# Performance work log

Measured on AMD Instinct MI355X. Metric: run time of the kernel, lower is better.

The kernel has to match this reference:

```python
import jax, jax.numpy as jnp
import numpy as np

B = 1024          # batch of users
N_ITEMS = 100000  # catalog size
N_CLUSTERS = 10   # __init__ default num_clusters
D = 64            # low-rank dim of the inner recommender


def setup_inputs() -> dict:
    key = jax.random.key(0)
    k1, k2, k3, k4 = jax.random.split(key, 4)
    input_array = jax.random.uniform(k1, (B, N_CLUSTERS), dtype=jnp.float32)
    # partition of items into clusters (dense form of cluster_to_items / item_to_cluster)
    item_cluster = jax.random.randint(k2, (N_ITEMS,), 0, N_CLUSTERS, dtype=jnp.int64 if jax.config.jax_enable_x64 else jnp.int32)
    W1 = jax.random.normal(k3, (N_ITEMS, D), dtype=jnp.float32) * 0.02
    W2 = jax.random.normal(k4, (D, N_ITEMS), dtype=jnp.float32) * 0.02
    return {"input_array": input_array, "item_cluster": item_cluster, "W1": W1, "W2": W2}


def reference(input_array, item_cluster, W1, W2):
    # scatter cluster score to every item in the cluster == gather by item's cluster id
    user_vector = input_array[:, item_cluster]                 # [B, N_ITEMS]
    logits = (user_vector @ W1) @ W2                           # inner recommender, [B, N_ITEMS]
    probs = jax.nn.softmax(logits, axis=1)                     # [B, N_ITEMS]
    # per-user, per-cluster mean of item probabilities (segment mean over items)
    counts = jax.ops.segment_sum(jnp.ones((item_cluster.shape[0],), probs.dtype),
                                 item_cluster, num_segments=N_CLUSTERS)  # [N_CLUSTERS]
    sums = jax.ops.segment_sum(probs.T, item_cluster, num_segments=N_CLUSTERS).T  # [B, N_CLUSTERS]
    return sums / jnp.maximum(counts, 1.0)[None, :]            # empty cluster -> 0.0, as in source
```

## Files before the change

### kernel.cpp

```cpp
#include <hip/hip_runtime.h>
#include <hip/hip_bf16.h>

#define N_B 1024
#define N_ITEMS 100000
#define N_CLUSTERS 10
#define N_D 64
#define MAXT 6272
#define K1B 392
#define W2PB 1563
#define K3BY 48
#define NGW 192

typedef __attribute__((ext_vector_type(8))) short short8;
typedef __attribute__((ext_vector_type(4))) float f32x4;

#if defined(__has_builtin)
#if __has_builtin(__builtin_amdgcn_exp2f)
#define EXP2F(x) __builtin_amdgcn_exp2f(x)
#endif
#endif
#ifndef EXP2F
#define EXP2F(x) exp2f(x)
#endif

#define MFMA(a, b, c) __builtin_amdgcn_mfma_f32_16x16x32_bf16(a, b, c, 0, 0, 0)

__device__ __forceinline__ unsigned short bf16_rne(float x) {
  unsigned u = __float_as_uint(x);
  u += 0x7FFFu + ((u >> 16) & 1u);
  return (unsigned short)(u >> 16);
}
__device__ __forceinline__ float bf16_f(unsigned short b) {
  return __uint_as_float(((unsigned)b) << 16);
}

__global__ __launch_bounds__(256) void kA(
    const int* __restrict__ cl, const float* __restrict__ W1,
    const float* __restrict__ W2, float* __restrict__ S1p,
    float* __restrict__ cntp, int* __restrict__ inv,
    unsigned short* __restrict__ W2Ph, unsigned short* __restrict__ W2Pl) {
  __shared__ float smem[64 * 65];
  int t = threadIdx.x;
  if (blockIdx.x < K1B) {
    float (*s1)[N_CLUSTERS][N_D] = (float (*)[N_CLUSTERS][N_D])smem;
    float (*scnt)[N_CLUSTERS] =
        (float (*)[N_CLUSTERS])(smem + 4 * N_CLUSTERS * N_D);
    int wave = t >> 6, lane = t & 63;

    inv[blockIdx.x * 256 + t] = 0;

    float a[N_CLUSTERS], cn[N_CLUSTERS];
#pragma unroll
    for (int k = 0; k < N_CLUSTERS; ++k) { a[k] = 0.f; cn[k] = 0.f; }

    int gw = blockIdx.x * 4 + wave;
    int r0 = gw * 64;
#pragma unroll 1
    for (int b = 0; b < 8; ++b) {
      int i0 = r0 + b * 8;
      float w[8];
      int c[8];
      if (i0 + 8 <= N_ITEMS) {
#pragma unroll
        for (int j = 0; j < 8; ++j) {
          c[j] = cl[i0 + j];
          w[j] = W1[(size_t)(i0 + j) * N_D + lane];
        }
      } else {
#pragma unroll
        for (int j = 0; j < 8; ++j) {
          int i = i0 + j;
          bool ok = i < N_ITEMS;
          c[j] = ok ? cl[i] : -1;
          w[j] = ok ? W1[(size_t)i * N_D + lane] : 0.f;
        }
      }
#pragma unroll
      for (int j = 0; j < 8; ++j)
#pragma unroll
        for (int k = 0; k < N_CLUSTERS; ++k) {
          bool m = (c[j] == k);
          a[k] += m ? w[j] : 0.f;
          cn[k] += m ? 1.f : 0.f;
        }
    }
#pragma unroll
    for (int k = 0; k < N_CLUSTERS; ++k) s1[wave][k][lane] = a[k];
    if (lane == 0) {
#pragma unroll
      for (int k = 0; k < N_CLUSTERS; ++k) scnt[wave][k] = cn[k];
    }
    __syncthreads();
    const float* fs1 = smem;
    for (int i = t; i < N_CLUSTERS * N_D; i += 256) {
      S1p[blockIdx.x * 640 + i] =
          fs1[i] + fs1[640 + i] + fs1[1280 + i] + fs1[1920 + i];
    }
    if (t < N_CLUSTERS) {
      cntp[blockIdx.x * N_CLUSTERS + t] =
          scnt[0][t] + scnt[1][t] + scnt[2][t] + scnt[3][t];
    }
  } else {
    float (*tile)[65] = (float (*)[65])smem;
    int blk = blockIdx.x - K1B;
    int c0 = blk * 64;
    int cl_ = t & 63;
    int r0 = t >> 6;
    bool okr = (c0 + cl_) < N_ITEMS;
#pragma unroll
    for (int rr = 0; rr < 16; ++rr) {
      int r = rr * 4 + r0;
      tile[cl_][r] = okr ? W2[(size_t)r * N_ITEMS + c0 + cl_] : 0.f;
    }
    __syncthreads();
#pragma unroll
    for (int itw = 0; itw < 8; ++itw) {
      int task = itw * 256 + t;
      int c_l = task >> 5, dp = task & 31;
      int c = c0 + c_l;
      if (c < N_ITEMS) {
        float v0 = tile[c_l][dp * 2], v1 = tile[c_l][dp * 2 + 1];
        unsigned short h0 = bf16_rne(v0), h1 = bf16_rne(v1);
        unsigned short l0 = bf16_rne(v0 - bf16_f(h0));
        unsigned short l1 = bf16_rne(v1 - bf16_f(h1));
        ((unsigned*)W2Ph)[(size_t)c * 32 + dp] =
            (unsigned)h0 | ((unsigned)h1 << 16);
        ((unsigned*)W2Pl)[(size_t)c * 32 + dp] =
            (unsigned)l0 | ((unsigned)l1 << 16);
      }
    }
  }
}

__global__ __launch_bounds__(256) void k1r(
    const float* __restrict__ S1p, const float* __restrict__ cntp,
    float* __restrict__ S1g, float* __restrict__ cntF, int* __restrict__ meta,
    int* __restrict__ tinfo, int* __restrict__ cursor) {
  int t = threadIdx.x;
  if (blockIdx.x > 0) {
    __shared__ float sgp[4][64];
    int wave = t >> 6, lane = t & 63;
    int col = (blockIdx.x - 1) * 64 + lane;
    float s = 0.f;
    const float* sp = S1p + col;
#pragma unroll 4
    for (int b = wave; b < K1B; b += 4) s += sp[b * 640];
    sgp[wave][lane] = s;
    __syncthreads();
    if (t < 64) {
      S1g[(blockIdx.x - 1) * 64 + t] =
          sgp[0][t] + sgp[1][t] + sgp[2][t] + sgp[3][t];
    }
    return;
  }
  __shared__ int baseS[11];
  __shared__ int cntI[N_CLUSTERS];
  __shared__ float part[16][N_CLUSTERS];
  if (t < 16) cursor[t] = 0;
  if (t < 160) {
    int c = t % N_CLUSTERS, g = t / N_CLUSTERS;
    float s = 0.f;
    for (int b = g; b < K1B; b += 16) s += cntp[b * N_CLUSTERS + c];
    part[g][c] = s;
  }
  __syncthreads();
  if (t < N_CLUSTERS) {
    float s = 0.f;
#pragma unroll
    for (int g = 0; g < 16; ++g) s += part[g][t];
    cntF[t] = s;
    cntI[t] = (int)(s + 0.5f);
  }
  __syncthreads();
  if (t == 0) {
    int acc = 0;
    for (int c = 0; c < N_CLUSTERS; ++c) {
      baseS[c] = acc;
      acc += ((cntI[c] + 15) >> 4) << 4;
    }
    baseS[10] = acc;
    for (int c = 0; c < 11; ++c) meta[c] = baseS[c];
    meta[11] = acc >> 4;
  }
  __syncthreads();
  int NT = baseS[10] >> 4;
  for (int jt = t; jt < MAXT; jt += 256) {
    int c = 0, nv = 0;
    if (jt < NT) {
      int p0 = jt * 16;
      for (int k = 0; k < N_CLUSTERS; ++k)
        if (p0 >= baseS[k] && p0 < baseS[k + 1]) c = k;
      nv = min(16, cntI[c] - (p0 - baseS[c]));
      if (nv < 0) nv = 0;
    }
    tinfo[jt] = c | (nv << 8);
  }
}

__global__ __launch_bounds__(256) void kB(
    const int* __restrict__ cl, const int* __restrict__ meta,
    int* __restrict__ cursor, int* __restrict__ inv,
    const float* __restrict__ inp, const float* __restrict__ S1g,
    short8* __restrict__ hfrag, float* __restrict__ bucket) {
  __shared__ int wn[4][N_CLUSTERS];
  __shared__ int bb[N_CLUSTERS];
  int t = threadIdx.x;
  if (blockIdx.x < 391) {
    int i = blockIdx.x * 256 + t;
    if (i < N_B * N_CLUSTERS) bucket[i] = 0.f;
    int wave = t >> 6, lane = t & 63;
    int c = (i < N_ITEMS) ? cl[i] : -1;
    unsigned long long m[N_CLUSTERS];
#pragma unroll
    for (int k = 0; k < N_CLUSTERS; ++k) {
      m[k] = __ballot(c == k);
      if (lane == 0) wn[wave][k] = __popcll(m[k]);
    }
    __syncthreads();
    if (t < N_CLUSTERS) {
      int tot = wn[0][t] + wn[1][t] + wn[2][t] + wn[3][t];
      bb[t] = tot ? atomicAdd(&cursor[t], tot) : 0;
    }
    __syncthreads();
    if (c >= 0) {
      int rank = 0;
#pragma unroll
      for (int k = 0; k < N_CLUSTERS; ++k)
        if (c == k) rank = __popcll(m[k] & ((1ull << lane) - 1ull));
      int wsum = 0;
      for (int w2 = 0; w2 < wave; ++w2) wsum += wn[w2][c];
      inv[meta[c] + bb[c] + wsum + rank] = i;
    }
  } else {
    int id = (blockIdx.x - 391) * 256 + t;
    int lane = id & 63;
    int ks = (id >> 6) & 1;
    int rt = (id >> 7) & 3;
    int bx = id >> 9;
    int row = bx * 64 + rt * 16 + (lane & 15);
    int d0 = ks * 32 + (lane >> 4) * 8;
    float hv[8];
#pragma unroll
    for (int j = 0; j < 8; ++j) hv[j] = 0.f;
#pragma unroll
    for (int c = 0; c < N_CLUSTERS; ++c) {
      float ic = inp[row * N_CLUSTERS + c];
      const float* sp = S1g + c * N_D + d0;
#pragma unroll
      for (int j = 0; j < 8; ++j) hv[j] += ic * sp[j];
    }
    short8 hi8, lo8;
#pragma unroll
    for (int j = 0; j < 8; ++j) {
      float x = hv[j] * 1.44269504088896340736f;
      unsigned short us = bf16_rne(x);
      hi8[j] = (short)us;
      lo8[j] = (short)bf16_rne(x - bf16_f(us));
    }
    int f0 = rt * 4 + ks * 2;
    hfrag[(bx * 16 + f0) * 64 + lane] = hi8;
    hfrag[(bx * 16 + f0 + 1) * 64 + lane] = lo8;
  }
}

__global__ __launch_bounds__(256, 3) void k3_mfma(
    const unsigned short* __restrict__ W2Ph,
    const unsigned short* __restrict__ W2Pl,
    const short8* __restrict__ hfrag, const int* __restrict__ inv,
    const int* __restrict__ tinfo, float* __restrict__ bucket) {
  __shared__ int linv[4][544];
  int t = threadIdx.x;
  int wave = t >> 6, lane = t & 63;
  int l15 = lane & 15, quad = lane >> 4;

  int lid = blockIdx.y * 16 + blockIdx.x;
  int nid = (lid & 7) * 96 + (lid >> 3);
  int bx = nid & 15, by = nid >> 4;

  int gw = by * 4 + wave;
  int jt0 = (MAXT * gw) / NGW;
  int nt = (MAXT * (gw + 1)) / NGW - jt0;

  short8 fr[16];
  {
    const short8* hp = hfrag + bx * 1024 + lane;
#pragma unroll
    for (int f = 0; f < 16; ++f) fr[f] = hp[f * 64];
  }
  int tiv = tinfo[jt0 + ((lane < nt) ? lane : nt - 1)];
  {
    const int* ip = inv + jt0 * 16;
    int n = nt * 16;
    for (int i = lane; i < n; i += 64) linv[wave][i] = ip[i];
  }
  __syncthreads();

  f32x4 acc[4];
#pragma unroll
  for (int r = 0; r < 4; ++r) acc[r] = (f32x4){0.f, 0.f, 0.f, 0.f};

  short8 xh0, xl0, xh1, xl1, yh0, yl0, yh1, yl1;
  int cc, nv, colN;
  {
    int c0 = inv[jt0 * 16 + l15];
    int o = c0 * 64 + quad * 8;
    xh0 = *(const short8*)(W2Ph + o);
    xh1 = *(const short8*)(W2Ph + o + 32);
    xl0 = *(const short8*)(W2Pl + o);
    xl1 = *(const short8*)(W2Pl + o + 32);
    colN = inv[jt0 * 16 + 16 + l15];
    int ti = __builtin_amdgcn_readlane(tiv, 0);
    cc = ti & 255;
    nv = ti >> 8;
  }

#define K3_FLUSH()                                                            \
  {                                                                           \
    _Pragma("unroll") for (int rt = 0; rt < 4; ++rt) {                        \
      float e0 = acc[rt][0], e1 = acc[rt][1];                                 \
      float e2 = acc[rt][2], e3 = acc[rt][3];                                 \
      _Pragma("unroll") for (int mm = 1; mm < 16; mm <<= 1) {                 \
        e0 += __shfl_xor(e0, mm, 64);                                         \
        e1 += __shfl_xor(e1, mm, 64);                                         \
        e2 += __shfl_xor(e2, mm, 64);                                         \
        e3 += __shfl_xor(e3, mm, 64);                                         \
      }                                                                       \
      if (l15 == 0) {                                                         \
        int r = bx * 64 + rt * 16 + quad * 4;                                 \
        atomicAdd(&bucket[(r + 0) * N_CLUSTERS + cc], e0);                    \
        atomicAdd(&bucket[(r + 1) * N_CLUSTERS + cc], e1);                    \
        atomicAdd(&bucket[(r + 2) * N_CLUSTERS + cc], e2);                    \
        atomicAdd(&bucket[(r + 3) * N_CLUSTERS + cc], e3);                    \
      }                                                                       \
      acc[rt] = (f32x4){0.f, 0.f, 0.f, 0.f};                                  \
    }                                                                         \
  }

#define K3_PHASE(CH0, CL0, CH1, CL1, NH0, NL0, NH1, NL1)                      \
  {                                                                           \
    int tin = __builtin_amdgcn_readlane(tiv, (it + 1 < nt) ? it + 1 : nt - 1);\
    int ccn = tin & 255, nvn = tin >> 8;                                      \
    {                                                                         \
      int o = colN * 64 + quad * 8;                   \
      NH0 = *(const short8*)(W2Ph + o);                                       \
      NH1 = *(const short8*)(W2Ph + o + 32);                                  \
      NL0 = *(const short8*)(W2Pl + o);                                       \
      NL1 = *(const short8*)(W2Pl + o + 32);                                  \
    }                                                                         \
    colN = linv[wave][((it + 2 < nt) ? it + 2 : nt - 1) * 16 + l15];          \
    f32x4 cr[4];                                                              \
    _Pragma("unroll") for (int rt = 0; rt < 4; ++rt) {                        \
      f32x4 c = {0.f, 0.f, 0.f, 0.f};                                         \
      c = MFMA(fr[rt * 4 + 0], CH0, c);                                       \
      c = MFMA(fr[rt * 4 + 0], CL0, c);                                       \
      c = MFMA(fr[rt * 4 + 1], CH0, c);                                       \
      c = MFMA(fr[rt * 4 + 2], CH1, c);                                       \
      c = MFMA(fr[rt * 4 + 2], CL1, c);                                       \
      c = MFMA(fr[rt * 4 + 3], CH1, c);                                       \
      cr[rt] = c;                                                             \
    }                                                                         \
    if (nv == 16) {                                                           \
      _Pragma("unroll") for (int rt = 0; rt < 4; ++rt) {                      \
        acc[rt][0] += EXP2F(cr[rt][0]);                                       \
        acc[rt][1] += EXP2F(cr[rt][1]);                                       \
        acc[rt][2] += EXP2F(cr[rt][2]);                                       \
        acc[rt][3] += EXP2F(cr[rt][3]);                                       \
      }                                                                       \
    } else {                                                                  \
      _Pragma("unroll") for (int rt = 0; rt < 4; ++rt) {                      \
        acc[rt][0] += (l15 < nv) ? EXP2F(cr[rt][0]) : 0.f;                    \
        acc[rt][1] += (l15 < nv) ? EXP2F(cr[rt][1]) : 0.f;                    \
        acc[rt][2] += (l15 < nv) ? EXP2F(cr[rt][2]) : 0.f;                    \
        acc[rt][3] += (l15 < nv) ? EXP2F(cr[rt][3]) : 0.f;                    \
      }                                                                       \
    }                                                                         \
    if (it == nt - 1 || ccn != cc) K3_FLUSH();                                \
    cc = ccn;                                                                 \
    nv = nvn;                                                                 \
    ++it;                                                                     \
    if (it == nt) break;                                                      \
  }

  int it = 0;
  while (true) {
    K3_PHASE(xh0, xl0, xh1, xl1, yh0, yl0, yh1, yl1)
    K3_PHASE(yh0, yl0, yh1, yl1, xh0, xl0, xh1, xl1)
  }
#undef K3_PHASE
#undef K3_FLUSH
}

__global__ __launch_bounds__(320) void k4_fin(
    const float* __restrict__ bucket, const float* __restrict__ cntF,
    float* __restrict__ out) {
  __shared__ float bl[32][N_CLUSTERS];
  int t = threadIdx.x;
  int r = t / N_CLUSTERS, c = t % N_CLUSTERS;
  int row = blockIdx.x * 32 + r;
  float s = bucket[row * N_CLUSTERS + c];
  bl[r][c] = s;
  __syncthreads();
  float tot = 0.f;
#pragma unroll
  for (int k = 0; k < N_CLUSTERS; ++k) tot += bl[r][k];
  out[row * N_CLUSTERS + c] = s / (tot * fmaxf(cntF[c], 1.f));
}

extern "C" void kernel_launch(void* const* d_in, const int* in_sizes, int n_in,
                              void* d_out, int out_size, void* d_ws, size_t ws_size,
                              hipStream_t stream) {
  const float* input = (const float*)d_in[0];
  const int* cl      = (const int*)d_in[1];
  const float* W1    = (const float*)d_in[2];
  const float* W2    = (const float*)d_in[3];
  float* out = (float*)d_out;
  float* ws = (float*)d_ws;

  float* S1g            = ws;
  float* cntF           = ws + 640;
  int*   meta           = (int*)(ws + 656);
  int*   cursor         = (int*)(ws + 672);
  int*   tinfo          = (int*)(ws + 1024);
  int*   inv            = (int*)(ws + 16384);
  short8* hfrag         = (short8*)(ws + 131072);
  unsigned short* W2Ph  = (unsigned short*)(ws + 262144);
  unsigned short* W2Pl  = (unsigned short*)(ws + 3463168);
  float* S1p            = ws + 6664192;
  float* cntp           = ws + 6915072;
  float* bucket         = ws + 6918992;

  kA<<<K1B + W2PB, 256, 0, stream>>>(cl, W1, W2, S1p, cntp, inv, W2Ph, W2Pl);
  k1r<<<11, 256, 0, stream>>>(S1p, cntp, S1g, cntF, meta, tinfo, cursor);
  kB<<<391 + 32, 256, 0, stream>>>(cl, meta, cursor, inv, input, S1g, hfrag,
                                   bucket);
  dim3 g3(16, K3BY);
  k3_mfma<<<g3, 256, 0, stream>>>(W2Ph, W2Pl, hfrag, inv, tinfo, bucket);
  k4_fin<<<32, 320, 0, stream>>>(bucket, cntF, out);
}
```

Before: 179.2 us.

## Hand-schedule W2 prefetch loads with inline asm and explicit vmcnt waits

```diff
diff --git a/kernel.cpp b/kernel.cpp
--- a/kernel.cpp
+++ b/kernel.cpp
@@ -295,20 +295,28 @@
   }
   __syncthreads();
 
+#pragma unroll
+  for (int f = 0; f < 16; ++f) asm volatile("" ::"v"(fr[f]));
+  asm volatile("" ::"v"(tiv));
+
   f32x4 acc[4];
 #pragma unroll
   for (int r = 0; r < 4; ++r) acc[r] = (f32x4){0.f, 0.f, 0.f, 0.f};
 
-  short8 xh0, xl0, xh1, xl1, yh0, yl0, yh1, yl1;
+  short8 xh0, xh1, xl0, xl1, yh0, yh1, yl0, yl1;
   int cc, nv, colN;
   {
-    int c0 = inv[jt0 * 16 + l15];
-    int o = c0 * 64 + quad * 8;
-    xh0 = *(const short8*)(W2Ph + o);
-    xh1 = *(const short8*)(W2Ph + o + 32);
-    xl0 = *(const short8*)(W2Pl + o);
-    xl1 = *(const short8*)(W2Pl + o + 32);
-    colN = inv[jt0 * 16 + 16 + l15];
+    int c0 = linv[wave][l15];
+    const unsigned short* ph = W2Ph + (size_t)c0 * 64 + quad * 8;
+    const unsigned short* pl = W2Pl + (size_t)c0 * 64 + quad * 8;
+    asm volatile(
+        "global_load_dwordx4 %0, %4, off\n\t"
+        "global_load_dwordx4 %1, %4, off offset:64\n\t"
+        "global_load_dwordx4 %2, %5, off\n\t"
+        "global_load_dwordx4 %3, %5, off offset:64"
+        : "=&v"(xh0), "=&v"(xh1), "=&v"(xl0), "=&v"(xl1)
+        : "v"(ph), "v"(pl));
+    colN = linv[wave][16 + l15];
     int ti = __builtin_amdgcn_readlane(tiv, 0);
     cc = ti & 255;
     nv = ti >> 8;
@@ -341,13 +349,20 @@
     int tin = __builtin_amdgcn_readlane(tiv, (it + 1 < nt) ? it + 1 : nt - 1);\
     int ccn = tin & 255, nvn = tin >> 8;                                      \
     {                                                                         \
-      int o = colN * 64 + quad * 8;                   \
-      NH0 = *(const short8*)(W2Ph + o);                                       \
-      NH1 = *(const short8*)(W2Ph + o + 32);                                  \
-      NL0 = *(const short8*)(W2Pl + o);                                       \
-      NL1 = *(const short8*)(W2Pl + o + 32);                                  \
+      const unsigned short* ph = W2Ph + (size_t)colN * 64 + quad * 8;         \
+      const unsigned short* pl = W2Pl + (size_t)colN * 64 + quad * 8;         \
+      asm volatile(                                                           \
+          "global_load_dwordx4 %0, %4, off\n\t"                               \
+          "global_load_dwordx4 %1, %4, off offset:64\n\t"                     \
+          "global_load_dwordx4 %2, %5, off\n\t"                               \
+          "global_load_dwordx4 %3, %5, off offset:64"                         \
+          : "=&v"(NH0), "=&v"(NH1), "=&v"(NL0), "=&v"(NL1)                    \
+          : "v"(ph), "v"(pl));                                                \
     }                                                                         \
     colN = linv[wave][((it + 2 < nt) ? it + 2 : nt - 1) * 16 + l15];          \
+    asm volatile("s_waitcnt vmcnt(4)" ::: "memory");                          \
+    __builtin_amdgcn_sched_barrier(0);                                        \
+    __builtin_amdgcn_s_setprio(1);                                            \
     f32x4 cr[4];                                                              \
     _Pragma("unroll") for (int rt = 0; rt < 4; ++rt) {                        \
       f32x4 c = {0.f, 0.f, 0.f, 0.f};                                         \
@@ -359,6 +374,7 @@
       c = MFMA(fr[rt * 4 + 3], CH1, c);                                       \
       cr[rt] = c;                                                             \
     }                                                                         \
+    __builtin_amdgcn_s_setprio(0);                                            \
     if (nv == 16) {                                                           \
       _Pragma("unroll") for (int rt = 0; rt < 4; ++rt) {                      \
         acc[rt][0] += EXP2F(cr[rt][0]);                                       \
```

New measurement: 180.6 us. No clear change (+0.8%).

## Fuse launches via last-block tickets and compute h fragments inside MFMA kernel

Applied to the files above, without the earlier changes.

```diff
diff --git a/kernel.cpp b/kernel.cpp
--- a/kernel.cpp
+++ b/kernel.cpp
@@ -8,6 +8,7 @@
 #define MAXT 6272
 #define K1B 392
 #define W2PB 1563
+#define NBLK3 768
 #define K3BY 48
 #define NGW 192
 
@@ -38,8 +39,12 @@
     const int* __restrict__ cl, const float* __restrict__ W1,
     const float* __restrict__ W2, float* __restrict__ S1p,
     float* __restrict__ cntp, int* __restrict__ inv,
-    unsigned short* __restrict__ W2Ph, unsigned short* __restrict__ W2Pl) {
+    unsigned short* __restrict__ W2Ph, unsigned short* __restrict__ W2Pl,
+    float* __restrict__ cntF, int* __restrict__ meta,
+    int* __restrict__ tinfo, int* __restrict__ cursor,
+    int* __restrict__ segdone) {
   __shared__ float smem[64 * 65];
+  __shared__ int ticket;
   int t = threadIdx.x;
   if (blockIdx.x < K1B) {
     float (*s1)[N_CLUSTERS][N_D] = (float (*)[N_CLUSTERS][N_D])smem;
@@ -99,6 +104,56 @@
     if (t < N_CLUSTERS) {
       cntp[blockIdx.x * N_CLUSTERS + t] =
           scnt[0][t] + scnt[1][t] + scnt[2][t] + scnt[3][t];
+    }
+    __threadfence();
+    __syncthreads();
+    if (t == 0) ticket = atomicAdd(segdone, 1);
+    __syncthreads();
+    if (ticket == K1B - 1) {
+      __threadfence();
+      __shared__ int baseS[11];
+      __shared__ int cntI[N_CLUSTERS];
+      float (*part)[N_CLUSTERS] = (float (*)[N_CLUSTERS])smem;
+      if (t < 16) cursor[t] = 0;
+      if (t < 160) {
+        int c = t % N_CLUSTERS, g = t / N_CLUSTERS;
+        float s = 0.f;
+        for (int b2 = g; b2 < K1B; b2 += 16) s += cntp[b2 * N_CLUSTERS + c];
+        part[g][c] = s;
+      }
+      __syncthreads();
+      if (t < N_CLUSTERS) {
+        float s = 0.f;
+#pragma unroll
+        for (int g = 0; g < 16; ++g) s += part[g][t];
+        cntF[t] = s;
+        cntI[t] = (int)(s + 0.5f);
+      }
+      __syncthreads();
+      if (t == 0) {
+        int acc = 0;
+        for (int c = 0; c < N_CLUSTERS; ++c) {
+          baseS[c] = acc;
+          acc += ((cntI[c] + 15) >> 4) << 4;
+        }
+        baseS[10] = acc;
+        for (int c = 0; c < 11; ++c) meta[c] = baseS[c];
+        meta[11] = acc >> 4;
+        *segdone = 0;
+      }
+      __syncthreads();
+      int NT = baseS[10] >> 4;
+      for (int jt = t; jt < MAXT; jt += 256) {
+        int c = 0, nv = 0;
+        if (jt < NT) {
+          int p0 = jt * 16;
+          for (int k = 0; k < N_CLUSTERS; ++k)
+            if (p0 >= baseS[k] && p0 < baseS[k + 1]) c = k;
+          nv = min(16, cntI[c] - (p0 - baseS[c]));
+          if (nv < 0) nv = 0;
+        }
+        tinfo[jt] = c | (nv << 8);
+      }
     }
   } else {
     float (*tile)[65] = (float (*)[65])smem;
@@ -132,143 +187,66 @@
   }
 }
 
-__global__ __launch_bounds__(256) void k1r(
-    const float* __restrict__ S1p, const float* __restrict__ cntp,
-    float* __restrict__ S1g, float* __restrict__ cntF, int* __restrict__ meta,
-    int* __restrict__ tinfo, int* __restrict__ cursor) {
+__global__ __launch_bounds__(256) void kX(
+    const int* __restrict__ cl, const int* __restrict__ meta,
+    int* __restrict__ cursor, int* __restrict__ inv,
+    const float* __restrict__ S1p, float* __restrict__ S1g,
+    float* __restrict__ bucket) {
   int t = threadIdx.x;
-  if (blockIdx.x > 0) {
+  int wave = t >> 6, lane = t & 63;
+  if (blockIdx.x < 10) {
     __shared__ float sgp[4][64];
-    int wave = t >> 6, lane = t & 63;
-    int col = (blockIdx.x - 1) * 64 + lane;
+    int col = blockIdx.x * 64 + lane;
     float s = 0.f;
     const float* sp = S1p + col;
 #pragma unroll 4
-    for (int b = wave; b < K1B; b += 4) s += sp[b * 640];
+    for (int b2 = wave; b2 < K1B; b2 += 4) s += sp[b2 * 640];
     sgp[wave][lane] = s;
     __syncthreads();
     if (t < 64) {
-      S1g[(blockIdx.x - 1) * 64 + t] =
+      S1g[blockIdx.x * 64 + t] =
           sgp[0][t] + sgp[1][t] + sgp[2][t] + sgp[3][t];
     }
     return;
   }
-  __shared__ int baseS[11];
-  __shared__ int cntI[N_CLUSTERS];
-  __shared__ float part[16][N_CLUSTERS];
-  if (t < 16) cursor[t] = 0;
-  if (t < 160) {
-    int c = t % N_CLUSTERS, g = t / N_CLUSTERS;
-    float s = 0.f;
-    for (int b = g; b < K1B; b += 16) s += cntp[b * N_CLUSTERS + c];
-    part[g][c] = s;
+  __shared__ int wn[4][N_CLUSTERS];
+  __shared__ int bb[N_CLUSTERS];
+  int vb = blockIdx.x - 10;
+  int i = vb * 256 + t;
+  if (i < N_B * N_CLUSTERS) bucket[i] = 0.f;
+  int c = (i < N_ITEMS) ? cl[i] : -1;
+  unsigned long long m[N_CLUSTERS];
+#pragma unroll
+  for (int k = 0; k < N_CLUSTERS; ++k) {
+    m[k] = __ballot(c == k);
+    if (lane == 0) wn[wave][k] = __popcll(m[k]);
   }
   __syncthreads();
   if (t < N_CLUSTERS) {
-    float s = 0.f;
-#pragma unroll
-    for (int g = 0; g < 16; ++g) s += part[g][t];
-    cntF[t] = s;
-    cntI[t] = (int)(s + 0.5f);
+    int tot = wn[0][t] + wn[1][t] + wn[2][t] + wn[3][t];
+    bb[t] = tot ? atomicAdd(&cursor[t], tot) : 0;
   }
   __syncthreads();
-  if (t == 0) {
-    int acc = 0;
-    for (int c = 0; c < N_CLUSTERS; ++c) {
-      baseS[c] = acc;
-      acc += ((cntI[c] + 15) >> 4) << 4;
-    }
-    baseS[10] = acc;
-    for (int c = 0; c < 11; ++c) meta[c] = baseS[c];
-    meta[11] = acc >> 4;
-  }
-  __syncthreads();
-  int NT = baseS[10] >> 4;
-  for (int jt = t; jt < MAXT; jt += 256) {
-    int c = 0, nv = 0;
-    if (jt < NT) {
-      int p0 = jt * 16;
-      for (int k = 0; k < N_CLUSTERS; ++k)
-        if (p0 >= baseS[k] && p0 < baseS[k + 1]) c = k;
-      nv = min(16, cntI[c] - (p0 - baseS[c]));
-      if (nv < 0) nv = 0;
-    }
-    tinfo[jt] = c | (nv << 8);
-  }
-}
-
-__global__ __launch_bounds__(256) void kB(
-    const int* __restrict__ cl, const int* __restrict__ meta,
-    int* __restrict__ cursor, int* __restrict__ inv,
-    const float* __restrict__ inp, const float* __restrict__ S1g,
-    short8* __restrict__ hfrag, float* __restrict__ bucket) {
-  __shared__ int wn[4][N_CLUSTERS];
-  __shared__ int bb[N_CLUSTERS];
-  int t = threadIdx.x;
-  if (blockIdx.x < 391) {
-    int i = blockIdx.x * 256 + t;
-    if (i < N_B * N_CLUSTERS) bucket[i] = 0.f;
-    int wave = t >> 6, lane = t & 63;
-    int c = (i < N_ITEMS) ? cl[i] : -1;
-    unsigned long long m[N_CLUSTERS];
-#pragma unroll
-    for (int k = 0; k < N_CLUSTERS; ++k) {
-      m[k] = __ballot(c == k);
-      if (lane == 0) wn[wave][k] = __popcll(m[k]);
-    }
-    __syncthreads();
-    if (t < N_CLUSTERS) {
-      int tot = wn[0][t] + wn[1][t] + wn[2][t] + wn[3][t];
-      bb[t] = tot ? atomicAdd(&cursor[t], tot) : 0;
-    }
-    __syncthreads();
-    if (c >= 0) {
-      int rank = 0;
-#pragma unroll
-      for (int k = 0; k < N_CLUSTERS; ++k)
-        if (c == k) rank = __popcll(m[k] & ((1ull << lane) - 1ull));
-      int wsum = 0;
-      for (int w2 = 0; w2 < wave; ++w2) wsum += wn[w2][c];
-      inv[meta[c] + bb[c] + wsum + rank] = i;
-    }
-  } else {
-    int id = (blockIdx.x - 391) * 256 + t;
-    int lane = id & 63;
-    int ks = (id >> 6) & 1;
-    int rt = (id >> 7) & 3;
-    int bx = id >> 9;
-    int row = bx * 64 + rt * 16 + (lane & 15);
-    int d0 = ks * 32 + (lane >> 4) * 8;
-    float hv[8];
-#pragma unroll
-    for (int j = 0; j < 8; ++j) hv[j] = 0.f;
-#pragma unroll
-    for (int c = 0; c < N_CLUSTERS; ++c) {
-      float ic = inp[row * N_CLUSTERS + c];
-      const float* sp = S1g + c * N_D + d0;
-#pragma unroll
-      for (int j = 0; j < 8; ++j) hv[j] += ic * sp[j];
-    }
-    short8 hi8, lo8;
-#pragma unroll
-    for (int j = 0; j < 8; ++j) {
-      float x = hv[j] * 1.44269504088896340736f;
-      unsigned short us = bf16_rne(x);
-      hi8[j] = (short)us;
-      lo8[j] = (short)bf16_rne(x - bf16_f(us));
-    }
-    int f0 = rt * 4 + ks * 2;
-    hfrag[(bx * 16 + f0) * 64 + lane] = hi8;
-    hfrag[(bx * 16 + f0 + 1) * 64 + lane] = lo8;
+  if (c >= 0) {
+    int rank = 0;
+#pragma unroll
+    for (int k = 0; k < N_CLUSTERS; ++k)
+      if (c == k) rank = __popcll(m[k] & ((1ull << lane) - 1ull));
+    int wsum = 0;
+    for (int w2 = 0; w2 < wave; ++w2) wsum += wn[w2][c];
+    inv[meta[c] + bb[c] + wsum + rank] = i;
   }
 }
 
 __global__ __launch_bounds__(256, 3) void k3_mfma(
     const unsigned short* __restrict__ W2Ph,
     const unsigned short* __restrict__ W2Pl,
-    const short8* __restrict__ hfrag, const int* __restrict__ inv,
-    const int* __restrict__ tinfo, float* __restrict__ bucket) {
+    const float* __restrict__ inp, const float* __restrict__ S1g,
+    const int* __restrict__ inv, const int* __restrict__ tinfo,
+    float* __restrict__ bucket, const float* __restrict__ cntF,
+    float* __restrict__ out, int* __restrict__ k3done) {
   __shared__ int linv[4][544];
+  __shared__ int tk;
   int t = threadIdx.x;
   int wave = t >> 6, lane = t & 63;
   int l15 = lane & 15, quad = lane >> 4;
@@ -281,18 +259,41 @@
   int jt0 = (MAXT * gw) / NGW;
   int nt = (MAXT * (gw + 1)) / NGW - jt0;
 
-  short8 fr[16];
-  {
-    const short8* hp = hfrag + bx * 1024 + lane;
-#pragma unroll
-    for (int f = 0; f < 16; ++f) fr[f] = hp[f * 64];
-  }
-  int tiv = tinfo[jt0 + ((lane < nt) ? lane : nt - 1)];
   {
     const int* ip = inv + jt0 * 16;
     int n = nt * 16;
     for (int i = lane; i < n; i += 64) linv[wave][i] = ip[i];
   }
+  short8 fr[16];
+#pragma unroll
+  for (int rt = 0; rt < 4; ++rt) {
+#pragma unroll
+    for (int ks = 0; ks < 2; ++ks) {
+      int row = bx * 64 + rt * 16 + (lane & 15);
+      int d0 = ks * 32 + (lane >> 4) * 8;
+      float hv[8];
+#pragma unroll
+      for (int j = 0; j < 8; ++j) hv[j] = 0.f;
+#pragma unroll
+      for (int c = 0; c < N_CLUSTERS; ++c) {
+        float ic = inp[row * N_CLUSTERS + c];
+        const float* sp = S1g + c * N_D + d0;
+#pragma unroll
+        for (int j = 0; j < 8; ++j) hv[j] += ic * sp[j];
+      }
+      short8 hi8, lo8;
+#pragma unroll
+      for (int j = 0; j < 8; ++j) {
+        float x = hv[j] * 1.44269504088896340736f;
+        unsigned short us = bf16_rne(x);
+        hi8[j] = (short)us;
+        lo8[j] = (short)bf16_rne(x - bf16_f(us));
+      }
+      fr[rt * 4 + ks * 2] = hi8;
+      fr[rt * 4 + ks * 2 + 1] = lo8;
+    }
+  }
+  int tiv = tinfo[jt0 + ((lane < nt) ? lane : nt - 1)];
   __syncthreads();
 
   f32x4 acc[4];
@@ -388,22 +389,23 @@
   }
 #undef K3_PHASE
 #undef K3_FLUSH
-}
-
-__global__ __launch_bounds__(320) void k4_fin(
-    const float* __restrict__ bucket, const float* __restrict__ cntF,
-    float* __restrict__ out) {
-  __shared__ float bl[32][N_CLUSTERS];
-  int t = threadIdx.x;
-  int r = t / N_CLUSTERS, c = t % N_CLUSTERS;
-  int row = blockIdx.x * 32 + r;
-  float s = bucket[row * N_CLUSTERS + c];
-  bl[r][c] = s;
+
+  __threadfence();
   __syncthreads();
-  float tot = 0.f;
-#pragma unroll
-  for (int k = 0; k < N_CLUSTERS; ++k) tot += bl[r][k];
-  out[row * N_CLUSTERS + c] = s / (tot * fmaxf(cntF[c], 1.f));
+  if (t == 0) tk = atomicAdd(k3done, 1);
+  __syncthreads();
+  if (tk == NBLK3 - 1) {
+    __threadfence();
+    for (int i = t; i < N_B * N_CLUSTERS; i += 256) {
+      int row = i / N_CLUSTERS, c = i % N_CLUSTERS;
+      float s = bucket[i];
+      float tot = 0.f;
+#pragma unroll
+      for (int k = 0; k < N_CLUSTERS; ++k) tot += bucket[row * N_CLUSTERS + k];
+      out[i] = s / (tot * fmaxf(cntF[c], 1.f));
+    }
+    if (t == 0) *k3done = 0;
+  }
 }
 
 extern "C" void kernel_launch(void* const* d_in, const int* in_sizes, int n_in,
@@ -420,20 +422,22 @@
   float* cntF           = ws + 640;
   int*   meta           = (int*)(ws + 656);
   int*   cursor         = (int*)(ws + 672);
+  int*   segdone        = (int*)(ws + 688);
+  int*   k3done         = (int*)(ws + 689);
   int*   tinfo          = (int*)(ws + 1024);
   int*   inv            = (int*)(ws + 16384);
-  short8* hfrag         = (short8*)(ws + 131072);
   unsigned short* W2Ph  = (unsigned short*)(ws + 262144);
   unsigned short* W2Pl  = (unsigned short*)(ws + 3463168);
   float* S1p            = ws + 6664192;
   float* cntp           = ws + 6915072;
   float* bucket         = ws + 6918992;
 
-  kA<<<K1B + W2PB, 256, 0, stream>>>(cl, W1, W2, S1p, cntp, inv, W2Ph, W2Pl);
-  k1r<<<11, 256, 0, stream>>>(S1p, cntp, S1g, cntF, meta, tinfo, cursor);
-  kB<<<391 + 32, 256, 0, stream>>>(cl, meta, cursor, inv, input, S1g, hfrag,
-                                   bucket);
+  hipMemsetAsync((char*)d_ws + 688 * 4, 0, 8, stream);
+
+  kA<<<K1B + W2PB, 256, 0, stream>>>(cl, W1, W2, S1p, cntp, inv, W2Ph, W2Pl,
+                                     cntF, meta, tinfo, cursor, segdone);
+  kX<<<401, 256, 0, stream>>>(cl, meta, cursor, inv, S1p, S1g, bucket);
   dim3 g3(16, K3BY);
-  k3_mfma<<<g3, 256, 0, stream>>>(W2Ph, W2Pl, hfrag, inv, tinfo, bucket);
-  k4_fin<<<32, 320, 0, stream>>>(bucket, cntF, out);
-}
+  k3_mfma<<<g3, 256, 0, stream>>>(W2Ph, W2Pl, input, S1g, inv, tinfo, bucket,
+                                  cntF, out, k3done);
+}
```

Result: slower. 294.0 us (+64.0%).
